# Performance work log

Hardware: AMD Instinct MI355X
Metric: run time of the kernel (lower is better)

The kernel has to match this reference:

```python
import jax, jax.numpy as jnp
import numpy as np

MAX_ITER = 3  # matches init max_iter
# structures exercised: sib_be, sib_bb, cop, grd, split (all distinct branches)


def _mfvi(s_const, s_arg_begin, s_arg_end,
          s_sib_be, s_sib_eb, s_sib_bb, s_sib_ee,
          s_cop_b, s_cop_e, s_grd_b, s_grd_e, s_split,
          edge_mask, chart_mask):
    B, S, _ = edge_mask.shape
    idx = jnp.arange(S)
    hs = jnp.broadcast_to(idx[:, None], (S, S))   # hs[i,j] = i (head index)
    ms = jnp.broadcast_to(idx[None, :], (S, S))   # ms[i,j] = j (modifier index)
    ls, rs = jnp.minimum(hs, ms), jnp.maximum(hs, ms)

    c0 = chart_mask[:, 0]
    pad_mask = c0[:, :, None] & c0[:, None, :]           # [B,j,k]
    chart = jnp.roll(chart_mask, 1, axis=1)              # cat((chart[:,-1:], chart[:,:-1]), 1)

    # [B,i,j,k] = edge[b,i,j] & edge[b,i,k]
    mask2o_base = edge_mask[:, :, :, None] & edge_mask[:, :, None, :]
    ne_hk = (hs[:, :, None] != idx)                      # i != k
    mask2o_wm = mask2o_base & ne_hk[None]
    mask2o = mask2o_wm & (ms[:, :, None] != idx)[None]   # additionally j != k

    lhs = ls[None, :, :] >= hs[:, :, None]               # min(j,k) >= i
    rhs = rs[None, :, :] <= hs[:, :, None]               # max(j,k) <= i
    triu_jk = idx[:, None] <= idx[None, :]               # keep k >= j (torch .triu())
    noncross = mask2o_wm & (triu_jk[None, None] & (lhs | rhs)[None])

    span_m2o = (chart[:, :, :, None]
                & (rs[:, :, None] != idx)[None]          # max(i,j) != k
                & pad_mask[:, None, :, :])
    inside = (hs[:, :, None] <= idx) & (ms[:, :, None] >= idx)  # i<=k<=... & j>=k
    outside = (~inside)[None] & span_m2o

    mzero = lambda s, m: jnp.where(m, s, 0.0)
    s_sib_be_m = mzero(s_sib_be, mask2o_wm)
    s_sib_eb_m = mzero(s_sib_eb, jnp.swapaxes(mask2o_wm, -2, -1))
    s_sib_bb_m = mzero(s_sib_bb, mask2o)
    s_sib_ee_m = mzero(s_sib_ee, mask2o)
    s_cop_b_m = mzero(s_cop_b, mask2o)
    s_cop_e_m = mzero(s_cop_e, mask2o)
    s_edge_grd_b = mzero(s_grd_b, noncross)
    s_edge_grd_e = mzero(s_grd_e, jnp.swapaxes(noncross, -2, -1))
    s_span_grd_b = mzero(jnp.transpose(s_grd_b, (0, 2, 3, 1)), outside)
    s_span_grd_e = mzero(jnp.transpose(s_grd_e, (0, 3, 2, 1)), outside)
    s_split_m = mzero(s_split, span_m2o)

    # NOTE: the torch code does `tmp_q_b = s_arg_begin; tmp_q_b += ...`, which
    # mutates the base score tensors in place, so messages ACCUMULATE into the
    # bases across iterations. We reproduce that semantics here.
    base_b, base_e, base_s = s_arg_begin, s_arg_end, s_const
    q_b, q_e, q_s = base_b, base_e, base_s
    for _ in range(MAX_ITER):
        qb = jax.nn.sigmoid(q_b)
        qe = jax.nn.sigmoid(q_e)
        qs = jax.nn.sigmoid(q_s)
        base_b = (base_b
                  + jnp.einsum('bik,bijk->bij', qe, s_sib_be_m)
                  + jnp.einsum('bik,bijk->bij', qb, s_sib_bb_m)
                  + jnp.einsum('bkj,bijk->bij', qb, s_cop_b_m)
                  + jnp.einsum('bjk,bijk->bij', qs, s_edge_grd_b))
        base_e = (base_e
                  + jnp.einsum('bik,bijk->bij', qb, s_sib_eb_m)
                  + jnp.einsum('bik,bijk->bij', qe, s_sib_ee_m)
                  + jnp.einsum('bkj,bijk->bij', qe, s_cop_e_m)
                  + jnp.einsum('bkj,bijk->bij', qs, s_edge_grd_e))
        base_s = (base_s
                  + jnp.einsum('bki,bijk->bij', qb, s_span_grd_b)
                  + jnp.einsum('bkj,bijk->bij', qe, s_span_grd_e)
                  + jnp.einsum('bik,bijk->bij', qs, s_split_m))
        q_b, q_e, q_s = base_b, base_e, base_s
    return q_b, q_e, q_s


def setup_inputs() -> dict:
    key = jax.random.key(0)
    B, S = 4, 128
    ks = jax.random.split(key, 16)
    f3 = lambda k: jax.random.normal(k, (B, S, S), jnp.float32)
    # scale 4D scores down so sums over S stay in a sane sigmoid range
    f4 = lambda k: jax.random.normal(k, (B, S, S, S), jnp.float32) * 0.05
    return {
        's_const': f3(ks[0]),
        's_arg_begin': f3(ks[1]),
        's_arg_end': f3(ks[2]),
        's_sib_be': f4(ks[3]),
        's_sib_eb': f4(ks[4]),
        's_sib_bb': f4(ks[5]),
        's_sib_ee': f4(ks[6]),
        's_cop_b': f4(ks[7]),
        's_cop_e': f4(ks[8]),
        's_grd_b': f4(ks[9]),
        's_grd_e': f4(ks[10]),
        's_split': f4(ks[11]),
        'arg_begin_mask': jax.random.bernoulli(ks[12], 0.5, (B, S, S)),
        'chart_mask': jax.random.bernoulli(ks[13], 0.5, (B, S, S)),
    }


def reference(s_const, s_arg_begin, s_arg_end,
              s_sib_be, s_sib_eb, s_sib_bb, s_sib_ee,
              s_cop_b, s_cop_e, s_grd_b, s_grd_e, s_split,
              arg_begin_mask, chart_mask):
    return _mfvi(s_const, s_arg_begin, s_arg_end,
                 s_sib_be, s_sib_eb, s_sib_bb, s_sib_ee,
                 s_cop_b, s_cop_e, s_grd_b, s_grd_e, s_split,
                 arg_begin_mask, chart_mask)
```

## Files before the change

kernel.cpp:

```cpp
#include <hip/hip_runtime.h>

#define BB 4
#define S 128
#define SS (S*S)
#define BSS (BB*SS)
#define JSPLIT 4
#define ISPLIT 2

__device__ __forceinline__ int off3(int b, int i, int j) { return (b * S + i) * S + j; }
__device__ __forceinline__ int off4(int b, int i, int j, int k) { return ((b * S + i) * S + j) * S + k; }

__global__ __launch_bounds__(128) void k_sigmoid(const float* __restrict__ base,
                                                 float* __restrict__ ws) {
    int bi = blockIdx.x;
    int b = bi >> 7, i = bi & (S - 1);
    int j = threadIdx.x;
#pragma unroll
    for (int t = 0; t < 3; ++t) {
        float x = base[t * BSS + off3(b, i, j)];
        float q = 1.0f / (1.0f + expf(-x));
        ws[t * BSS + off3(b, i, j)] = q;
        ws[(3 + t) * BSS + off3(b, j, i)] = q;
    }
}

__global__ __launch_bounds__(256) void k_sib(
    const float* __restrict__ be, const float* __restrict__ bb,
    const float* __restrict__ cb, const float* __restrict__ eb,
    const float* __restrict__ ee, const float* __restrict__ ce,
    const float* __restrict__ sp, const int* __restrict__ edge,
    const int* __restrict__ chart, const float* __restrict__ ws,
    float* __restrict__ base) {
    const int b = blockIdx.z, I = blockIdx.y;
    const int jbase = blockIdx.x * (S / JSPLIT);
    const int t = threadIdx.x, w = t >> 6, l = t & 63;
    const int k0 = 2 * l, k1 = 2 * l + 1;

    const float* qb = ws;
    const float* qe = ws + BSS;
    const float* qs = ws + 2 * BSS;
    const float* qbT = ws + 3 * BSS;
    const float* qeT = ws + 4 * BSS;

    const int2 e_k = *(const int2*)&edge[off3(b, I, k0)];
    const float2 qe_i = *(const float2*)&qe[off3(b, I, k0)];
    const float2 qb_i = *(const float2*)&qb[off3(b, I, k0)];
    const float2 qs_i = *(const float2*)&qs[off3(b, I, k0)];
    const int2 c0k = *(const int2*)&chart[off3(b, 0, k0)];
    const int Iprev = (I + S - 1) & (S - 1);
    const bool ek0 = e_k.x != 0, ek1 = e_k.y != 0;
    const bool c0k0 = c0k.x != 0, c0k1 = c0k.y != 0;

    for (int jj = 0; jj < (S / JSPLIT) / 4; ++jj) {
        const int j = jbase + w + 4 * jj;
        const bool e_ij = edge[off3(b, I, j)] != 0;
        const bool chIj = chart[off3(b, Iprev, j)] != 0;
        const bool c0j = chart[off3(b, 0, j)] != 0;
        const float2 qbT_j = *(const float2*)&qbT[off3(b, j, k0)];
        const float2 qeT_j = *(const float2*)&qeT[off3(b, j, k0)];

        const int b4 = off4(b, I, j, 0);
        const float2 v_be = *(const float2*)&be[b4 + k0];
        const float2 v_bb = *(const float2*)&bb[b4 + k0];
        const float2 v_cb = *(const float2*)&cb[b4 + k0];
        const float2 v_eb = *(const float2*)&eb[b4 + k0];
        const float2 v_ee = *(const float2*)&ee[b4 + k0];
        const float2 v_ce = *(const float2*)&ce[b4 + k0];
        const float2 v_sp = *(const float2*)&sp[b4 + k0];

        const int mx = I > j ? I : j;
        const bool wmk = e_ij && (I != j);

        bool wm0 = e_ij && ek0 && (I != k0);
        bool m20 = wm0 && (j != k0);
        bool wk0 = ek0 && wmk;
        bool sp0 = chIj && (mx != k0) && c0j && c0k0;
        float accB = (wm0 ? qe_i.x : 0.f) * v_be.x + (m20 ? qb_i.x : 0.f) * v_bb.x +
                     (m20 ? qbT_j.x : 0.f) * v_cb.x;
        float accE = (wk0 ? qb_i.x : 0.f) * v_eb.x + (m20 ? qe_i.x : 0.f) * v_ee.x +
                     (m20 ? qeT_j.x : 0.f) * v_ce.x;
        float accS = (sp0 ? qs_i.x : 0.f) * v_sp.x;
        bool wm1 = e_ij && ek1 && (I != k1);
        bool m21 = wm1 && (j != k1);
        bool wk1 = ek1 && wmk;
        bool sp1 = chIj && (mx != k1) && c0j && c0k1;
        accB += (wm1 ? qe_i.y : 0.f) * v_be.y + (m21 ? qb_i.y : 0.f) * v_bb.y +
                (m21 ? qbT_j.y : 0.f) * v_cb.y;
        accE += (wk1 ? qb_i.y : 0.f) * v_eb.y + (m21 ? qe_i.y : 0.f) * v_ee.y +
                (m21 ? qeT_j.y : 0.f) * v_ce.y;
        accS += (sp1 ? qs_i.y : 0.f) * v_sp.y;

#pragma unroll
        for (int o = 32; o > 0; o >>= 1) {
            accB += __shfl_xor(accB, o);
            accE += __shfl_xor(accE, o);
            accS += __shfl_xor(accS, o);
        }
        if (l == 0) {
            atomicAdd(&base[0 * BSS + off3(b, I, j)], accB);
            atomicAdd(&base[1 * BSS + off3(b, I, j)], accE);
            atomicAdd(&base[2 * BSS + off3(b, I, j)], accS);
        }
    }
}

__global__ __launch_bounds__(256) void k_grd(
    const float* __restrict__ gb, const float* __restrict__ ge,
    const int* __restrict__ edge, const int* __restrict__ chart,
    const float* __restrict__ ws, float* __restrict__ base) {
    const int b = blockIdx.z, J = blockIdx.y;
    const int is = blockIdx.x;
    const int t = threadIdx.x, h = t >> 6, l = t & 63;
    const int K0 = 2 * l, K1 = 2 * l + 1;

    const float* qs = ws + 2 * BSS;
    const float* qbT = ws + 3 * BSS;
    const float* qeT = ws + 4 * BSS;
    const float* qsT = ws + 5 * BSS;

    const float2 qs_J = *(const float2*)&qs[off3(b, J, K0)];
    const float2 qsT_J = *(const float2*)&qsT[off3(b, J, K0)];
    const int2 c0Kv = *(const int2*)&chart[off3(b, 0, K0)];
    const bool c0K0 = c0Kv.x != 0, c0K1 = c0Kv.y != 0;
    const bool c0J = chart[off3(b, 0, J)] != 0;
    const int Jprev = (J + S - 1) & (S - 1);
    const int2 chJKv = *(const int2*)&chart[off3(b, Jprev, K0)];
    const bool chJK0 = chJKv.x != 0, chJK1 = chJKv.y != 0;
    const bool chKJ0 = chart[off3(b, (K0 + S - 1) & (S - 1), J)] != 0;
    const bool chKJ1 = chart[off3(b, K0, J)] != 0;
    const int mxJ0 = J > K0 ? J : K0;
    const int mxJ1 = J > K1 ? J : K1;

    float rs_b0 = 0.f, rs_b1 = 0.f, rs_e0 = 0.f, rs_e1 = 0.f;

    for (int ib = is * (32 / ISPLIT); ib < (is + 1) * (32 / ISPLIT); ++ib) {
        const int I = 4 * ib + h;
        const float2 v_b = *(const float2*)&gb[off4(b, I, J, K0)];
        const float2 v_e = *(const float2*)&ge[off4(b, I, J, K0)];
        const int2 e_IKv = *(const int2*)&edge[off3(b, I, K0)];
        const bool eIK0 = e_IKv.x != 0, eIK1 = e_IKv.y != 0;
        const bool eIJ = edge[off3(b, I, J)] != 0;
        const bool c0I = chart[off3(b, 0, I)] != 0;
        const float qbT_JI = qbT[off3(b, J, I)];
        const float qeT_JI = qeT[off3(b, J, I)];

        bool nc1_0 = eIJ && eIK0 && (I != K0) && (J <= K0) && (J >= I || K0 <= I);
        bool nc1_1 = eIJ && eIK1 && (I != K1) && (J <= K1) && (J >= I || K1 <= I);
        bool nc2_0 = eIK0 && eIJ && (I != J) && (K0 <= J) && (K0 >= I || J <= I);
        bool nc2_1 = eIK1 && eIJ && (I != J) && (K1 <= J) && (K1 >= I || J <= I);
        float pb = (nc1_0 ? qs_J.x : 0.f) * v_b.x + (nc1_1 ? qs_J.y : 0.f) * v_b.y;
        float pe = (nc2_0 ? qsT_J.x : 0.f) * v_e.x + (nc2_1 ? qsT_J.y : 0.f) * v_e.y;

        bool o1_0 = !((J <= I) && (K0 >= I)) && chJK0 && (mxJ0 != I) && c0K0 && c0I;
        bool o1_1 = !((J <= I) && (K1 >= I)) && chJK1 && (mxJ1 != I) && c0K1 && c0I;
        bool o2_0 = !((K0 <= I) && (J >= I)) && chKJ0 && (mxJ0 != I) && c0J && c0I;
        bool o2_1 = !((K1 <= I) && (J >= I)) && chKJ1 && (mxJ1 != I) && c0J && c0I;
        rs_b0 += (o1_0 ? qbT_JI : 0.f) * v_b.x;
        rs_b1 += (o1_1 ? qbT_JI : 0.f) * v_b.y;
        rs_e0 += (o2_0 ? qeT_JI : 0.f) * v_e.x;
        rs_e1 += (o2_1 ? qeT_JI : 0.f) * v_e.y;

#pragma unroll
        for (int o = 32; o > 0; o >>= 1) {
            pb += __shfl_xor(pb, o);
            pe += __shfl_xor(pe, o);
        }
        if (l == 0) {
            atomicAdd(&base[0 * BSS + off3(b, I, J)], pb);
            atomicAdd(&base[1 * BSS + off3(b, I, J)], pe);
        }
    }
    atomicAdd(&base[2 * BSS + off3(b, J, K0)], rs_b0);
    atomicAdd(&base[2 * BSS + off3(b, J, K1)], rs_b1);
    atomicAdd(&base[2 * BSS + off3(b, K0, J)], rs_e0);
    atomicAdd(&base[2 * BSS + off3(b, K1, J)], rs_e1);
}

extern "C" void kernel_launch(void* const* d_in, const int* in_sizes, int n_in,
                              void* d_out, int out_size, void* d_ws, size_t ws_size,
                              hipStream_t stream) {
    (void)in_sizes; (void)n_in; (void)out_size; (void)ws_size;
    const float* s_const = (const float*)d_in[0];
    const float* s_arg_begin = (const float*)d_in[1];
    const float* s_arg_end = (const float*)d_in[2];
    const float* be = (const float*)d_in[3];
    const float* eb = (const float*)d_in[4];
    const float* bb = (const float*)d_in[5];
    const float* ee = (const float*)d_in[6];
    const float* cb = (const float*)d_in[7];
    const float* ce = (const float*)d_in[8];
    const float* gb = (const float*)d_in[9];
    const float* ge = (const float*)d_in[10];
    const float* sp = (const float*)d_in[11];
    const int* edge = (const int*)d_in[12];
    const int* chart = (const int*)d_in[13];
    float* base = (float*)d_out;
    float* ws = (float*)d_ws;

    hipMemcpyAsync(base, s_arg_begin, BSS * sizeof(float), hipMemcpyDeviceToDevice, stream);
    hipMemcpyAsync(base + BSS, s_arg_end, BSS * sizeof(float), hipMemcpyDeviceToDevice, stream);
    hipMemcpyAsync(base + 2 * BSS, s_const, BSS * sizeof(float), hipMemcpyDeviceToDevice, stream);

    for (int it = 0; it < 3; ++it) {
        k_sigmoid<<<dim3(BB * S), dim3(S), 0, stream>>>(base, ws);
        k_sib<<<dim3(JSPLIT, S, BB), dim3(256), 0, stream>>>(be, bb, cb, eb, ee, ce, sp,
                                                             edge, chart, ws, base);
        k_grd<<<dim3(ISPLIT, S, BB), dim3(256), 0, stream>>>(gb, ge, edge, chart, ws, base);
    }
}
```

Measured before the change: 579.3 us.

## Fold initial copies into sigmoid, vectorize loads, replace atomics with plain stores

Drops the three device-to-device memcpys by having the first sigmoid launch read the input score tensors directly and write them into the output buffer. The sib and grd kernels now use float4 loads with half-wave (32-lane) reductions, so each wavefront handles two rows at once. The per-(I,j) atomics become read-modify-write stores, which is valid because each output element is owned by exactly one thread in each kernel. The grid split factors are doubled to keep enough blocks in flight. In k_grd the column-sum atomics are cut in half by combining the two half-waves with a shuffle first.

```diff
diff --git a/kernel.cpp b/kernel.cpp
--- a/kernel.cpp
+++ b/kernel.cpp
@@ -4,23 +4,28 @@
 #define S 128
 #define SS (S*S)
 #define BSS (BB*SS)
-#define JSPLIT 4
-#define ISPLIT 2
+#define JSPLIT 8
+#define ISPLIT 4
 
 __device__ __forceinline__ int off3(int b, int i, int j) { return (b * S + i) * S + j; }
 __device__ __forceinline__ int off4(int b, int i, int j, int k) { return ((b * S + i) * S + j) * S + k; }
 
-__global__ __launch_bounds__(128) void k_sigmoid(const float* __restrict__ base,
-                                                 float* __restrict__ ws) {
+__global__ __launch_bounds__(128) void k_sigmoid(const float* __restrict__ sb,
+                                                 const float* __restrict__ se,
+                                                 const float* __restrict__ ss,
+                                                 float* base,
+                                                 float* __restrict__ ws, int init) {
     int bi = blockIdx.x;
     int b = bi >> 7, i = bi & (S - 1);
     int j = threadIdx.x;
+    const float* src[3] = {sb, se, ss};
 #pragma unroll
     for (int t = 0; t < 3; ++t) {
-        float x = base[t * BSS + off3(b, i, j)];
+        float x = src[t][off3(b, i, j)];
         float q = 1.0f / (1.0f + expf(-x));
         ws[t * BSS + off3(b, i, j)] = q;
         ws[(3 + t) * BSS + off3(b, j, i)] = q;
+        if (init) base[t * BSS + off3(b, i, j)] = x;
     }
 }
 
@@ -34,7 +39,8 @@
     const int b = blockIdx.z, I = blockIdx.y;
     const int jbase = blockIdx.x * (S / JSPLIT);
     const int t = threadIdx.x, w = t >> 6, l = t & 63;
-    const int k0 = 2 * l, k1 = 2 * l + 1;
+    const int h = (l >> 5) & 1, lh = l & 31;
+    const int k = 4 * lh;
 
     const float* qb = ws;
     const float* qe = ws + BSS;
@@ -42,64 +48,70 @@
     const float* qbT = ws + 3 * BSS;
     const float* qeT = ws + 4 * BSS;
 
-    const int2 e_k = *(const int2*)&edge[off3(b, I, k0)];
-    const float2 qe_i = *(const float2*)&qe[off3(b, I, k0)];
-    const float2 qb_i = *(const float2*)&qb[off3(b, I, k0)];
-    const float2 qs_i = *(const float2*)&qs[off3(b, I, k0)];
-    const int2 c0k = *(const int2*)&chart[off3(b, 0, k0)];
+    const float4 qb_i = *(const float4*)&qb[off3(b, I, k)];
+    const float4 qe_i = *(const float4*)&qe[off3(b, I, k)];
+    const float4 qs_i = *(const float4*)&qs[off3(b, I, k)];
+    const int4 ekv = *(const int4*)&edge[off3(b, I, k)];
+    const int4 c0kv = *(const int4*)&chart[off3(b, 0, k)];
     const int Iprev = (I + S - 1) & (S - 1);
-    const bool ek0 = e_k.x != 0, ek1 = e_k.y != 0;
-    const bool c0k0 = c0k.x != 0, c0k1 = c0k.y != 0;
-
-    for (int jj = 0; jj < (S / JSPLIT) / 4; ++jj) {
-        const int j = jbase + w + 4 * jj;
+    bool ek[4], c0k[4];
+#pragma unroll
+    for (int c = 0; c < 4; ++c) {
+        ek[c] = (&ekv.x)[c] != 0;
+        c0k[c] = (&c0kv.x)[c] != 0;
+    }
+
+#pragma unroll
+    for (int it = 0; it < (S / JSPLIT) / 8; ++it) {
+        const int j = jbase + 8 * it + 2 * w + h;
+        const float ob_b = base[0 * BSS + off3(b, I, j)];
+        const float ob_e = base[1 * BSS + off3(b, I, j)];
+        const float ob_s = base[2 * BSS + off3(b, I, j)];
         const bool e_ij = edge[off3(b, I, j)] != 0;
         const bool chIj = chart[off3(b, Iprev, j)] != 0;
         const bool c0j = chart[off3(b, 0, j)] != 0;
-        const float2 qbT_j = *(const float2*)&qbT[off3(b, j, k0)];
-        const float2 qeT_j = *(const float2*)&qeT[off3(b, j, k0)];
-
-        const int b4 = off4(b, I, j, 0);
-        const float2 v_be = *(const float2*)&be[b4 + k0];
-        const float2 v_bb = *(const float2*)&bb[b4 + k0];
-        const float2 v_cb = *(const float2*)&cb[b4 + k0];
-        const float2 v_eb = *(const float2*)&eb[b4 + k0];
-        const float2 v_ee = *(const float2*)&ee[b4 + k0];
-        const float2 v_ce = *(const float2*)&ce[b4 + k0];
-        const float2 v_sp = *(const float2*)&sp[b4 + k0];
+        const float4 qbT_j = *(const float4*)&qbT[off3(b, j, k)];
+        const float4 qeT_j = *(const float4*)&qeT[off3(b, j, k)];
+
+        const int b4 = off4(b, I, j, k);
+        const float4 v_be = *(const float4*)&be[b4];
+        const float4 v_bb = *(const float4*)&bb[b4];
+        const float4 v_cb = *(const float4*)&cb[b4];
+        const float4 v_eb = *(const float4*)&eb[b4];
+        const float4 v_ee = *(const float4*)&ee[b4];
+        const float4 v_ce = *(const float4*)&ce[b4];
+        const float4 v_sp = *(const float4*)&sp[b4];
 
         const int mx = I > j ? I : j;
-        const bool wmk = e_ij && (I != j);
-
-        bool wm0 = e_ij && ek0 && (I != k0);
-        bool m20 = wm0 && (j != k0);
-        bool wk0 = ek0 && wmk;
-        bool sp0 = chIj && (mx != k0) && c0j && c0k0;
-        float accB = (wm0 ? qe_i.x : 0.f) * v_be.x + (m20 ? qb_i.x : 0.f) * v_bb.x +
-                     (m20 ? qbT_j.x : 0.f) * v_cb.x;
-        float accE = (wk0 ? qb_i.x : 0.f) * v_eb.x + (m20 ? qe_i.x : 0.f) * v_ee.x +
-                     (m20 ? qeT_j.x : 0.f) * v_ce.x;
-        float accS = (sp0 ? qs_i.x : 0.f) * v_sp.x;
-        bool wm1 = e_ij && ek1 && (I != k1);
-        bool m21 = wm1 && (j != k1);
-        bool wk1 = ek1 && wmk;
-        bool sp1 = chIj && (mx != k1) && c0j && c0k1;
-        accB += (wm1 ? qe_i.y : 0.f) * v_be.y + (m21 ? qb_i.y : 0.f) * v_bb.y +
-                (m21 ? qbT_j.y : 0.f) * v_cb.y;
-        accE += (wk1 ? qb_i.y : 0.f) * v_eb.y + (m21 ? qe_i.y : 0.f) * v_ee.y +
-                (m21 ? qeT_j.y : 0.f) * v_ce.y;
-        accS += (sp1 ? qs_i.y : 0.f) * v_sp.y;
-
-#pragma unroll
-        for (int o = 32; o > 0; o >>= 1) {
+        const bool wmj = e_ij && (I != j);
+
+        float accB = 0.f, accE = 0.f, accS = 0.f;
+#pragma unroll
+        for (int c = 0; c < 4; ++c) {
+            const int kc = k + c;
+            const bool wm = e_ij && ek[c] && (I != kc);
+            const bool m2 = wm && (j != kc);
+            const bool wk = ek[c] && wmj;
+            const bool spn = chIj && (mx != kc) && c0j && c0k[c];
+            accB += (wm ? (&qe_i.x)[c] : 0.f) * (&v_be.x)[c] +
+                    (m2 ? (&qb_i.x)[c] : 0.f) * (&v_bb.x)[c] +
+                    (m2 ? (&qbT_j.x)[c] : 0.f) * (&v_cb.x)[c];
+            accE += (wk ? (&qb_i.x)[c] : 0.f) * (&v_eb.x)[c] +
+                    (m2 ? (&qe_i.x)[c] : 0.f) * (&v_ee.x)[c] +
+                    (m2 ? (&qeT_j.x)[c] : 0.f) * (&v_ce.x)[c];
+            accS += (spn ? (&qs_i.x)[c] : 0.f) * (&v_sp.x)[c];
+        }
+
+#pragma unroll
+        for (int o = 16; o > 0; o >>= 1) {
             accB += __shfl_xor(accB, o);
             accE += __shfl_xor(accE, o);
             accS += __shfl_xor(accS, o);
         }
-        if (l == 0) {
-            atomicAdd(&base[0 * BSS + off3(b, I, j)], accB);
-            atomicAdd(&base[1 * BSS + off3(b, I, j)], accE);
-            atomicAdd(&base[2 * BSS + off3(b, I, j)], accS);
+        if (lh == 0) {
+            base[0 * BSS + off3(b, I, j)] = ob_b + accB;
+            base[1 * BSS + off3(b, I, j)] = ob_e + accE;
+            base[2 * BSS + off3(b, I, j)] = ob_s + accS;
         }
     }
 }
@@ -108,72 +120,86 @@
     const float* __restrict__ gb, const float* __restrict__ ge,
     const int* __restrict__ edge, const int* __restrict__ chart,
     const float* __restrict__ ws, float* __restrict__ base) {
-    const int b = blockIdx.z, J = blockIdx.y;
-    const int is = blockIdx.x;
-    const int t = threadIdx.x, h = t >> 6, l = t & 63;
-    const int K0 = 2 * l, K1 = 2 * l + 1;
+    const int b = blockIdx.z, J = blockIdx.y, is = blockIdx.x;
+    const int t = threadIdx.x, w = t >> 6, l = t & 63;
+    const int h = (l >> 5) & 1, lh = l & 31;
+    const int K = 4 * lh;
 
     const float* qs = ws + 2 * BSS;
     const float* qbT = ws + 3 * BSS;
     const float* qeT = ws + 4 * BSS;
     const float* qsT = ws + 5 * BSS;
 
-    const float2 qs_J = *(const float2*)&qs[off3(b, J, K0)];
-    const float2 qsT_J = *(const float2*)&qsT[off3(b, J, K0)];
-    const int2 c0Kv = *(const int2*)&chart[off3(b, 0, K0)];
-    const bool c0K0 = c0Kv.x != 0, c0K1 = c0Kv.y != 0;
+    const float4 qs_J = *(const float4*)&qs[off3(b, J, K)];
+    const float4 qsT_J = *(const float4*)&qsT[off3(b, J, K)];
+    const int4 c0Kv = *(const int4*)&chart[off3(b, 0, K)];
     const bool c0J = chart[off3(b, 0, J)] != 0;
     const int Jprev = (J + S - 1) & (S - 1);
-    const int2 chJKv = *(const int2*)&chart[off3(b, Jprev, K0)];
-    const bool chJK0 = chJKv.x != 0, chJK1 = chJKv.y != 0;
-    const bool chKJ0 = chart[off3(b, (K0 + S - 1) & (S - 1), J)] != 0;
-    const bool chKJ1 = chart[off3(b, K0, J)] != 0;
-    const int mxJ0 = J > K0 ? J : K0;
-    const int mxJ1 = J > K1 ? J : K1;
-
-    float rs_b0 = 0.f, rs_b1 = 0.f, rs_e0 = 0.f, rs_e1 = 0.f;
-
-    for (int ib = is * (32 / ISPLIT); ib < (is + 1) * (32 / ISPLIT); ++ib) {
-        const int I = 4 * ib + h;
-        const float2 v_b = *(const float2*)&gb[off4(b, I, J, K0)];
-        const float2 v_e = *(const float2*)&ge[off4(b, I, J, K0)];
-        const int2 e_IKv = *(const int2*)&edge[off3(b, I, K0)];
-        const bool eIK0 = e_IKv.x != 0, eIK1 = e_IKv.y != 0;
+    const int4 chJKv = *(const int4*)&chart[off3(b, Jprev, K)];
+    bool c0K[4], chJK[4], chKJ[4];
+    int mxJ[4];
+#pragma unroll
+    for (int c = 0; c < 4; ++c) {
+        c0K[c] = (&c0Kv.x)[c] != 0;
+        chJK[c] = (&chJKv.x)[c] != 0;
+        chKJ[c] = chart[off3(b, (K + c + S - 1) & (S - 1), J)] != 0;
+        mxJ[c] = J > (K + c) ? J : (K + c);
+    }
+
+    float rsb[4] = {0.f, 0.f, 0.f, 0.f}, rse[4] = {0.f, 0.f, 0.f, 0.f};
+
+#pragma unroll
+    for (int itI = 0; itI < (S / ISPLIT) / 8; ++itI) {
+        const int I = is * (S / ISPLIT) + 8 * itI + 2 * w + h;
+        const float ob0 = base[0 * BSS + off3(b, I, J)];
+        const float ob1 = base[1 * BSS + off3(b, I, J)];
+        const float4 v_b = *(const float4*)&gb[off4(b, I, J, K)];
+        const float4 v_e = *(const float4*)&ge[off4(b, I, J, K)];
+        const int4 eIKv = *(const int4*)&edge[off3(b, I, K)];
         const bool eIJ = edge[off3(b, I, J)] != 0;
         const bool c0I = chart[off3(b, 0, I)] != 0;
         const float qbT_JI = qbT[off3(b, J, I)];
         const float qeT_JI = qeT[off3(b, J, I)];
 
-        bool nc1_0 = eIJ && eIK0 && (I != K0) && (J <= K0) && (J >= I || K0 <= I);
-        bool nc1_1 = eIJ && eIK1 && (I != K1) && (J <= K1) && (J >= I || K1 <= I);
-        bool nc2_0 = eIK0 && eIJ && (I != J) && (K0 <= J) && (K0 >= I || J <= I);
-        bool nc2_1 = eIK1 && eIJ && (I != J) && (K1 <= J) && (K1 >= I || J <= I);
-        float pb = (nc1_0 ? qs_J.x : 0.f) * v_b.x + (nc1_1 ? qs_J.y : 0.f) * v_b.y;
-        float pe = (nc2_0 ? qsT_J.x : 0.f) * v_e.x + (nc2_1 ? qsT_J.y : 0.f) * v_e.y;
-
-        bool o1_0 = !((J <= I) && (K0 >= I)) && chJK0 && (mxJ0 != I) && c0K0 && c0I;
-        bool o1_1 = !((J <= I) && (K1 >= I)) && chJK1 && (mxJ1 != I) && c0K1 && c0I;
-        bool o2_0 = !((K0 <= I) && (J >= I)) && chKJ0 && (mxJ0 != I) && c0J && c0I;
-        bool o2_1 = !((K1 <= I) && (J >= I)) && chKJ1 && (mxJ1 != I) && c0J && c0I;
-        rs_b0 += (o1_0 ? qbT_JI : 0.f) * v_b.x;
-        rs_b1 += (o1_1 ? qbT_JI : 0.f) * v_b.y;
-        rs_e0 += (o2_0 ? qeT_JI : 0.f) * v_e.x;
-        rs_e1 += (o2_1 ? qeT_JI : 0.f) * v_e.y;
-
-#pragma unroll
-        for (int o = 32; o > 0; o >>= 1) {
+        float pb = 0.f, pe = 0.f;
+#pragma unroll
+        for (int c = 0; c < 4; ++c) {
+            const int Kc = K + c;
+            const bool eIK = (&eIKv.x)[c] != 0;
+            const float vb = (&v_b.x)[c], ve = (&v_e.x)[c];
+            const bool nc1 = eIJ && eIK && (I != Kc) && (J <= Kc) && (J >= I || Kc <= I);
+            const bool nc2 = eIK && eIJ && (I != J) && (Kc <= J) && (Kc >= I || J <= I);
+            pb += (nc1 ? (&qs_J.x)[c] : 0.f) * vb;
+            pe += (nc2 ? (&qsT_J.x)[c] : 0.f) * ve;
+            const bool o1 = !((J <= I) && (Kc >= I)) && chJK[c] && (mxJ[c] != I) && c0K[c] && c0I;
+            const bool o2 = !((Kc <= I) && (J >= I)) && chKJ[c] && (mxJ[c] != I) && c0J && c0I;
+            rsb[c] += (o1 ? qbT_JI : 0.f) * vb;
+            rse[c] += (o2 ? qeT_JI : 0.f) * ve;
+        }
+
+#pragma unroll
+        for (int o = 16; o > 0; o >>= 1) {
             pb += __shfl_xor(pb, o);
             pe += __shfl_xor(pe, o);
         }
-        if (l == 0) {
-            atomicAdd(&base[0 * BSS + off3(b, I, J)], pb);
-            atomicAdd(&base[1 * BSS + off3(b, I, J)], pe);
-        }
-    }
-    atomicAdd(&base[2 * BSS + off3(b, J, K0)], rs_b0);
-    atomicAdd(&base[2 * BSS + off3(b, J, K1)], rs_b1);
-    atomicAdd(&base[2 * BSS + off3(b, K0, J)], rs_e0);
-    atomicAdd(&base[2 * BSS + off3(b, K1, J)], rs_e1);
+        if (lh == 0) {
+            base[0 * BSS + off3(b, I, J)] = ob0 + pb;
+            base[1 * BSS + off3(b, I, J)] = ob1 + pe;
+        }
+    }
+
+#pragma unroll
+    for (int c = 0; c < 4; ++c) {
+        rsb[c] += __shfl_xor(rsb[c], 32);
+        rse[c] += __shfl_xor(rse[c], 32);
+    }
+    if (h == 0) {
+#pragma unroll
+        for (int c = 0; c < 4; ++c) {
+            atomicAdd(&base[2 * BSS + off3(b, J, K + c)], rsb[c]);
+            atomicAdd(&base[2 * BSS + off3(b, K + c, J)], rse[c]);
+        }
+    }
 }
 
 extern "C" void kernel_launch(void* const* d_in, const int* in_sizes, int n_in,
@@ -197,12 +223,13 @@
     float* base = (float*)d_out;
     float* ws = (float*)d_ws;
 
-    hipMemcpyAsync(base, s_arg_begin, BSS * sizeof(float), hipMemcpyDeviceToDevice, stream);
-    hipMemcpyAsync(base + BSS, s_arg_end, BSS * sizeof(float), hipMemcpyDeviceToDevice, stream);
-    hipMemcpyAsync(base + 2 * BSS, s_const, BSS * sizeof(float), hipMemcpyDeviceToDevice, stream);
-
     for (int it = 0; it < 3; ++it) {
-        k_sigmoid<<<dim3(BB * S), dim3(S), 0, stream>>>(base, ws);
+        if (it == 0)
+            k_sigmoid<<<dim3(BB * S), dim3(S), 0, stream>>>(s_arg_begin, s_arg_end, s_const,
+                                                            base, ws, 1);
+        else
+            k_sigmoid<<<dim3(BB * S), dim3(S), 0, stream>>>(base, base + BSS, base + 2 * BSS,
+                                                            base, ws, 0);
         k_sib<<<dim3(JSPLIT, S, BB), dim3(256), 0, stream>>>(be, bb, cb, eb, ee, ce, sp,
                                                              edge, chart, ws, base);
         k_grd<<<dim3(ISPLIT, S, BB), dim3(256), 0, stream>>>(gb, ge, edge, chart, ws, base);
```

Result: slower. 601.8 us (+3.9%).
